# Performance work log

Hardware: AMD Instinct MI355X
Metric: run time of the kernel (lower is better)

Reference implementation:

```python
import jax, jax.numpy as jnp
import numpy as np

B, F, D, L, N = 2048, 40, 64, 3, 40  # batch, num_fields, embed_dim, num_layers, num_subspaces


def setup_inputs() -> dict:
    key = jax.random.key(0)
    inputs = jax.random.normal(key, (B, F, D), dtype=jnp.float32)
    # Parameters per layer, matching torch init exactly:
    #   W     = identity(D) repeated over out_subspaces -> [N, D, D]
    #   alpha = ones([num_fields, in_subspaces, out_subspaces]); in_subspaces == F for
    #           layer 0 and == N afterwards; with N == F all layers share shape [F, N, N]
    #   h     = ones([N, D, 1])
    W = jnp.broadcast_to(jnp.eye(D, dtype=jnp.float32), (L, N, D, D)).copy()
    alpha = jnp.ones((L, F, N, N), dtype=jnp.float32)
    h = jnp.ones((L, N, D, 1), dtype=jnp.float32)
    return {"inputs": inputs, "W": W, "alpha": alpha, "h": h}


def _fusion_layer(B0, Bi, W, alpha, h):
    # Original math: fusion[b,n,D,d] = sum_{f,i} alpha[f,i,n] * B0[b,f,D] * Bi[b,i,d]
    #                out[b,n,D]     = sum_d fusion[b,n,D,d] * W[n,D,d] * h[n,d]
    # Reordered to avoid the [b,f,n,D,d] outer-product tensor:
    M = W * h[:, :, 0][:, None, :]                 # [n, D, d] = W * h broadcast over D
    C = jnp.einsum('bid,nDd->binD', Bi, M)         # contract embed dim d first
    out = jnp.einsum('bfD,fin,binD->bnD', B0, alpha, C)
    return out


def reference(inputs, W, alpha, h):
    B_i = inputs
    for l in range(L):
        B_i = _fusion_layer(inputs, B_i, W[l], alpha[l], h[l])
    return B_i
```

## Files before the change

kernel.cpp:

```cpp
#include <hip/hip_runtime.h>


typedef __bf16 bf16x8 __attribute__((ext_vector_type(8)));
typedef float  f32x16 __attribute__((ext_vector_type(16)));
typedef unsigned short us4 __attribute__((ext_vector_type(4)));

constexpr int BATCH = 2048;
constexpr int FDIM  = 40;
constexpr int DDIM  = 64;
constexpr int LAY   = 3;
constexpr int FPAD  = 48;
constexpr int APAD  = 56;
constexpr int NSPL  = 8;
constexpr int NPB   = FDIM / NSPL;
constexpr int BPB   = 8;
constexpr int MSLAB = DDIM * DDIM;
constexpr int ASLAB = DDIM * APAD;

__device__ __forceinline__ unsigned short f2bf(float f) {
  union { float f; unsigned u; } v; v.f = f;
  unsigned r = v.u + 0x7fff + ((v.u >> 16) & 1);
  return (unsigned short)(r >> 16);
}

__device__ __forceinline__ void dma16(unsigned short* lds, const unsigned short* g) {
  __builtin_amdgcn_global_load_lds(
      (const __attribute__((address_space(1))) unsigned int*)g,
      (__attribute__((address_space(3))) unsigned int*)lds, 16, 0, 0);
}

__global__ __launch_bounds__(256) void prep_all(
    const float* __restrict__ inputs, const float* __restrict__ W,
    const float* __restrict__ h, const float* __restrict__ alpha,
    unsigned short* __restrict__ B0b, unsigned short* __restrict__ B0T,
    unsigned short* __restrict__ M, unsigned short* __restrict__ AT) {
  __shared__ float lds[FDIM][DDIM + 1];
  if (blockIdx.x < BATCH) {
    const int b = blockIdx.x;
    const float* src = inputs + (size_t)b * FDIM * DDIM;
    for (int cch = threadIdx.x; cch < FDIM * DDIM / 4; cch += 256) {
      float4 v = reinterpret_cast<const float4*>(src)[cch];
      int e = cch * 4;
      int f = e >> 6, d = e & 63;
      lds[f][d] = v.x; lds[f][d + 1] = v.y; lds[f][d + 2] = v.z; lds[f][d + 3] = v.w;
      us4 o = { f2bf(v.x), f2bf(v.y), f2bf(v.z), f2bf(v.w) };
      reinterpret_cast<us4*>(B0b + (size_t)b * FDIM * DDIM)[cch] = o;
    }
    __syncthreads();
    for (int cch = threadIdx.x; cch < DDIM * FPAD / 4; cch += 256) {
      int f4 = cch % (FPAD / 4);
      int d  = cch / (FPAD / 4);
      us4 o = {0, 0, 0, 0};
      if (f4 < FDIM / 4) {
        int f = f4 * 4;
        o[0] = f2bf(lds[f][d]);     o[1] = f2bf(lds[f + 1][d]);
        o[2] = f2bf(lds[f + 2][d]); o[3] = f2bf(lds[f + 3][d]);
      }
      reinterpret_cast<us4*>(B0T + (size_t)b * DDIM * FPAD)[cch] = o;
    }
    return;
  }
  int j = (blockIdx.x - BATCH) * 256 + threadIdx.x;
  const int nM4  = LAY * FDIM * MSLAB / 4;
  const int nAl4 = LAY * FDIM * FDIM * FDIM / 4;
  if (j < nM4) {
    int e   = j * 4;
    int ln  = e >> 12;
    int row = (e >> 6) & 63;
    int jc  = (e >> 3) & 7;
    int o   = e & 7;
    int ds  = ((jc ^ (row & 7)) << 3) + o;
    float4 wv = *reinterpret_cast<const float4*>(W + ((size_t)ln * 64 + row) * 64 + ds);
    float4 hv = *reinterpret_cast<const float4*>(h + (size_t)ln * 64 + ds);
    us4 ov = { f2bf(wv.x * hv.x), f2bf(wv.y * hv.y), f2bf(wv.z * hv.z), f2bf(wv.w * hv.w) };
    *reinterpret_cast<us4*>(M + e) = ov;
    return;
  }
  j -= nM4;
  if (j >= nAl4) return;
  {
    int e = j * 4;
    int n = e % FDIM;
    int i = (e / FDIM) % FDIM;
    int f = (e / (FDIM * FDIM)) % FDIM;
    int l = e / (FDIM * FDIM * FDIM);
    float4 v = *reinterpret_cast<const float4*>(alpha + e);
    unsigned short* dst = AT + ((size_t)l * FDIM) * ASLAB + (size_t)i * APAD + f;
#pragma unroll
    for (int k = 0; k < 4; ++k) {
      float vk = (k == 0) ? v.x : (k == 1) ? v.y : (k == 2) ? v.z : v.w;
      dst[(size_t)(n + k) * ASLAB] = f2bf(vk);
    }
  }
}

template <bool FINAL>
__global__ __launch_bounds__(256, 2) void layer_k(
    const unsigned short* __restrict__ Bi,
    const unsigned short* __restrict__ B0T,
    const unsigned short* __restrict__ Mt,
    const unsigned short* __restrict__ ATt,
    void* __restrict__ outp)
{
  __shared__ unsigned short smM[2][MSLAB];
  __shared__ unsigned short smA[2][ASLAB];

  const int tid  = threadIdx.x;
  const int lane = tid & 63;
  const int w    = tid >> 6;
  const int c    = lane & 31;
  const int h    = lane >> 5;

  const int L  = (blockIdx.x & 7) * 256 + (blockIdx.x >> 3);
  const int bg = L >> 3;
  const int ns = L & 7;
  const int nBase = ns * NPB;
  const int bb = bg * BPB + w * 2;

  bf16x8 aBi[2][2][4];
#pragma unroll
  for (int b2 = 0; b2 < 2; ++b2)
#pragma unroll
    for (int it = 0; it < 2; ++it) {
      int row = it * 32 + c; if (row > FDIM - 1) row = FDIM - 1;
#pragma unroll
      for (int ks = 0; ks < 4; ++ks)
        aBi[b2][it][ks] = *reinterpret_cast<const bf16x8*>(
            Bi + ((size_t)(bb + b2) * FDIM + row) * DDIM + ks * 16 + h * 8);
    }
  bf16x8 bT[2][2][3];
#pragma unroll
  for (int b2 = 0; b2 < 2; ++b2)
#pragma unroll
    for (int dt = 0; dt < 2; ++dt)
#pragma unroll
      for (int ks = 0; ks < 3; ++ks)
        bT[b2][dt][ks] = *reinterpret_cast<const bf16x8*>(
            B0T + ((size_t)(bb + b2) * DDIM + dt * 32 + c) * FPAD + ks * 16 + h * 8);

  auto dmaChunk = [&](int nl, int bs) {
    const unsigned short* Ms = Mt  + (size_t)(nBase + nl) * MSLAB;
    const unsigned short* As = ATt + (size_t)(nBase + nl) * ASLAB;
#pragma unroll
    for (int r = 0; r < 2; ++r) {
      int k = tid + r * 256;
      dma16(&smM[bs][k * 8], Ms + k * 8);
    }
    dma16(&smA[bs][tid * 8], As + tid * 8);
    if (tid < 192) dma16(&smA[bs][(tid + 256) * 8], As + (tid + 256) * 8);
  };

  auto compute = [&](int nl, int bs) {
    const int n = nBase + nl;
    const unsigned short* mL = &smM[bs][0];
    const unsigned short* aL = &smA[bs][0];
    bf16x8 mb[2][4], at[2][3];
#pragma unroll
    for (int dt = 0; dt < 2; ++dt)
#pragma unroll
      for (int ks = 0; ks < 4; ++ks)
        mb[dt][ks] = *reinterpret_cast<const bf16x8*>(
            mL + (dt * 32 + c) * 64 + (((ks * 2 + h) ^ (c & 7)) * 8));
#pragma unroll
    for (int it = 0; it < 2; ++it)
#pragma unroll
      for (int ks = 0; ks < 3; ++ks)
        at[it][ks] = *reinterpret_cast<const bf16x8*>(
            aL + (it * 32 + c) * APAD + (ks * 2 + h) * 8);

    float pout[2][2] = {{0.f, 0.f}, {0.f, 0.f}};

    f32x16 cA, rA, cB, rB;

    auto issueT = [&](int b2, int dt, int it, f32x16& cc, f32x16& rr) {
      f32x16 c0 = {0,0,0,0,0,0,0,0,0,0,0,0,0,0,0,0};
      f32x16 r0 = {0,0,0,0,0,0,0,0,0,0,0,0,0,0,0,0};
#pragma unroll
      for (int ks = 0; ks < 3; ++ks) {
        c0 = __builtin_amdgcn_mfma_f32_32x32x16_bf16(aBi[b2][it][ks], mb[dt][ks], c0, 0, 0, 0);
        r0 = __builtin_amdgcn_mfma_f32_32x32x16_bf16(at[it][ks], bT[b2][dt][ks], r0, 0, 0, 0);
      }
      cc = __builtin_amdgcn_mfma_f32_32x32x16_bf16(aBi[b2][it][3], mb[dt][3], c0, 0, 0, 0);
      rr = r0;
    };
    auto combineT = [&](int b2, int dt, const f32x16& cc, const f32x16& rr) {
      float t0 = 0.f, t1 = 0.f, t2 = 0.f, t3 = 0.f;
#pragma unroll
      for (int r = 0; r < 4; ++r) {
        t0 += cc[r] * rr[r];         t1 += cc[r + 4] * rr[r + 4];
        t2 += cc[r + 8] * rr[r + 8]; t3 += cc[r + 12] * rr[r + 12];
      }
      pout[b2][dt] += (t0 + t1) + (t2 + t3);
    };

    issueT(0, 0, 0, cA, rA);
    issueT(1, 0, 0, cB, rB); combineT(0, 0, cA, rA);
    issueT(0, 1, 0, cA, rA); combineT(1, 0, cB, rB);
    issueT(1, 1, 0, cB, rB); combineT(0, 1, cA, rA);
    issueT(0, 0, 1, cA, rA); combineT(1, 1, cB, rB);
    issueT(1, 0, 1, cB, rB); combineT(0, 0, cA, rA);
    issueT(0, 1, 1, cA, rA); combineT(1, 0, cB, rB);
    issueT(1, 1, 1, cB, rB); combineT(0, 1, cA, rA);
    combineT(1, 1, cB, rB);

#pragma unroll
    for (int b2 = 0; b2 < 2; ++b2) {
      float v0 = pout[b2][0] + __shfl_xor(pout[b2][0], 32, 64);
      float v1 = pout[b2][1] + __shfl_xor(pout[b2][1], 32, 64);
      float val = h ? v1 : v0;
      size_t off = ((size_t)(bb + b2) * FDIM + n) * DDIM + lane;
      if (FINAL) ((float*)outp)[off] = val;
      else       ((unsigned short*)outp)[off] = f2bf(val);
    }
  };

  dmaChunk(0, 0);
  __syncthreads();
#pragma unroll 1
  for (int cc = 0; cc < NPB; ++cc) {
    const int bs = cc & 1;
    if (cc + 1 < NPB) dmaChunk(cc + 1, bs ^ 1);
    compute(cc, bs);
    __syncthreads();
  }
}

extern "C" void kernel_launch(void* const* d_in, const int* in_sizes, int n_in,
                              void* d_out, int out_size, void* d_ws, size_t ws_size,
                              hipStream_t stream) {
  const float* inputs = (const float*)d_in[0];
  const float* W      = (const float*)d_in[1];
  const float* alpha  = (const float*)d_in[2];
  const float* h      = (const float*)d_in[3];

  char* ws = (char*)d_ws;
  const size_t S   = (size_t)BATCH * FDIM * DDIM * 2;
  const size_t ST  = (size_t)BATCH * DDIM * FPAD * 2;
  unsigned short* Bi1 = (unsigned short*)(ws);
  unsigned short* Bi2 = (unsigned short*)(ws + S);
  unsigned short* B0b = (unsigned short*)(ws + 2 * S);
  unsigned short* B0T = (unsigned short*)(ws + 3 * S);
  unsigned short* Mb  = (unsigned short*)(ws + 3 * S + ST);
  unsigned short* ATb = (unsigned short*)(ws + 3 * S + ST + (size_t)LAY * FDIM * MSLAB * 2);

  hipMemsetAsync(ATb, 0, (size_t)LAY * FDIM * ASLAB * 2, stream);

  const int nPrep4 = (LAY * FDIM * MSLAB + LAY * FDIM * FDIM * FDIM) / 4;
  const int prepBlocks = BATCH + (nPrep4 + 255) / 256;
  prep_all<<<prepBlocks, 256, 0, stream>>>(inputs, W, h, alpha, B0b, B0T, Mb, ATb);

  dim3 grid(BATCH / BPB * NSPL), blk(256);
  const size_t mL = (size_t)FDIM * MSLAB;
  const size_t aL = (size_t)FDIM * ASLAB;
  layer_k<false><<<grid, blk, 0, stream>>>(B0b, B0T, Mb, ATb, Bi1);
  layer_k<false><<<grid, blk, 0, stream>>>(Bi1, B0T, Mb + mL, ATb + aL, Bi2);
  layer_k<true ><<<grid, blk, 0, stream>>>(Bi2, B0T, Mb + 2 * mL, ATb + 2 * aL, d_out);
}
```

Measured before the change: 253.7 us.

## Prefetch all per-block M and alpha slabs into LDS upfront

```diff
diff --git a/kernel.cpp b/kernel.cpp
--- a/kernel.cpp
+++ b/kernel.cpp
@@ -16,6 +16,7 @@
 constexpr int BPB   = 8;
 constexpr int MSLAB = DDIM * DDIM;
 constexpr int ASLAB = DDIM * APAD;
+constexpr int ALDS  = 4096;
 
 __device__ __forceinline__ unsigned short f2bf(float f) {
   union { float f; unsigned u; } v; v.f = f;
@@ -102,8 +103,8 @@
     const unsigned short* __restrict__ ATt,
     void* __restrict__ outp)
 {
-  __shared__ unsigned short smM[2][MSLAB];
-  __shared__ unsigned short smA[2][ASLAB];
+  __shared__ unsigned short smM[NPB][MSLAB];
+  __shared__ unsigned short smA[NPB][ALDS];
 
   const int tid  = threadIdx.x;
   const int lane = tid & 63;
@@ -117,6 +118,23 @@
   const int nBase = ns * NPB;
   const int bb = bg * BPB + w * 2;
 
+#pragma unroll
+  for (int nl = 0; nl < NPB; ++nl) {
+    const unsigned short* Ms = Mt  + (size_t)(nBase + nl) * MSLAB;
+    const unsigned short* As = ATt + (size_t)(nBase + nl) * ASLAB;
+#pragma unroll
+    for (int r = 0; r < 2; ++r) {
+      int k = tid + r * 256;
+      dma16(&smM[nl][k * 8], Ms + k * 8);
+    }
+#pragma unroll
+    for (int r = 0; r < 2; ++r) {
+      int k = tid + r * 256;
+      int ks = k < 447 ? k : 447;
+      dma16(&smA[nl][k * 8], As + ks * 8);
+    }
+  }
+
   bf16x8 aBi[2][2][4];
 #pragma unroll
   for (int b2 = 0; b2 < 2; ++b2)
@@ -138,22 +156,10 @@
         bT[b2][dt][ks] = *reinterpret_cast<const bf16x8*>(
             B0T + ((size_t)(bb + b2) * DDIM + dt * 32 + c) * FPAD + ks * 16 + h * 8);
 
-  auto dmaChunk = [&](int nl, int bs) {
-    const unsigned short* Ms = Mt  + (size_t)(nBase + nl) * MSLAB;
-    const unsigned short* As = ATt + (size_t)(nBase + nl) * ASLAB;
-#pragma unroll
-    for (int r = 0; r < 2; ++r) {
-      int k = tid + r * 256;
-      dma16(&smM[bs][k * 8], Ms + k * 8);
-    }
-    dma16(&smA[bs][tid * 8], As + tid * 8);
-    if (tid < 192) dma16(&smA[bs][(tid + 256) * 8], As + (tid + 256) * 8);
-  };
-
-  auto compute = [&](int nl, int bs) {
+  auto compute = [&](int nl) {
     const int n = nBase + nl;
-    const unsigned short* mL = &smM[bs][0];
-    const unsigned short* aL = &smA[bs][0];
+    const unsigned short* mL = &smM[nl][0];
+    const unsigned short* aL = &smA[nl][0];
     bf16x8 mb[2][4], at[2][3];
 #pragma unroll
     for (int dt = 0; dt < 2; ++dt)
@@ -214,15 +220,15 @@
     }
   };
 
-  dmaChunk(0, 0);
-  __syncthreads();
+  asm volatile("s_waitcnt vmcnt(16)" ::: "memory");
+  __builtin_amdgcn_s_barrier();
+  __builtin_amdgcn_sched_barrier(0);
+  compute(0);
+  asm volatile("s_waitcnt vmcnt(0)" ::: "memory");
+  __builtin_amdgcn_s_barrier();
+  __builtin_amdgcn_sched_barrier(0);
 #pragma unroll 1
-  for (int cc = 0; cc < NPB; ++cc) {
-    const int bs = cc & 1;
-    if (cc + 1 < NPB) dmaChunk(cc + 1, bs ^ 1);
-    compute(cc, bs);
-    __syncthreads();
-  }
+  for (int nl = 1; nl < NPB; ++nl) compute(nl);
 }
 
 extern "C" void kernel_launch(void* const* d_in, const int* in_sizes, int n_in,
```

Result: no change. 256.4 us (+1.1%).
